# Optimization experiments

Measured on AMD Instinct MI355X. Metric: run time of the kernel, lower is better.

The kernel has to match this reference:

```python
import jax, jax.numpy as jnp
import numpy as np

N_Q_HEADS = 16
N_KV_HEADS = 4
HEAD_DIM = 64
GROUPS = N_Q_HEADS // N_KV_HEADS


def apply_rope(xq, xk, cos, sin):
    # xq: [B,S,Hq,D], xk: [B,S,Hkv,D]; cos/sin: [S, D/2]
    def rot(t):
        tr = t[..., 0::2]
        ti = t[..., 1::2]
        c = cos[None, :, None, :]
        s = sin[None, :, None, :]
        out_r = tr * c - ti * s
        out_i = tr * s + ti * c
        # interleave back: [..., D/2, 2] -> [..., D]
        return jnp.stack([out_r, out_i], axis=-1).reshape(t.shape)
    return rot(xq), rot(xk)


def setup_inputs() -> dict:
    key = jax.random.key(0)
    ks = jax.random.split(key, 8)
    B, S, DIM = 2, 2048, 1024
    x = jax.random.normal(ks[0], (B, S, DIM), jnp.float32)
    # RoPE frequencies (llama-style): theta_i = 10000^(-2i/D), angles = pos * theta
    inv_freq = 1.0 / (10000.0 ** (jnp.arange(0, HEAD_DIM, 2, dtype=jnp.float32) / HEAD_DIM))
    angles = jnp.arange(S, dtype=jnp.float32)[:, None] * inv_freq[None, :]  # [S, D/2]
    freqs_cos = jnp.cos(angles)
    freqs_sin = jnp.sin(angles)
    # additive causal mask [1,1,S,S]
    neg = jnp.float32(-1e9)
    mask = jnp.where(jnp.tril(jnp.ones((S, S), bool)), 0.0, neg)[None, None]
    scale = 0.02
    wq = jax.random.normal(ks[1], (DIM, N_Q_HEADS * HEAD_DIM), jnp.float32) * scale
    wk = jax.random.normal(ks[2], (DIM, N_KV_HEADS * HEAD_DIM), jnp.float32) * scale
    wv = jax.random.normal(ks[3], (DIM, N_KV_HEADS * HEAD_DIM), jnp.float32) * scale
    wo = jax.random.normal(ks[4], (DIM, DIM), jnp.float32) * scale
    return {"x": x, "start_pos": 0, "freqs_cos": freqs_cos, "freqs_sin": freqs_sin,
            "mask": mask, "wq": wq, "wk": wk, "wv": wv, "wo": wo}


def reference(x, start_pos, freqs_cos, freqs_sin, mask, wq, wk, wv, wo):
    B, S, DIM = x.shape
    xq = (x @ wq).reshape(B, S, N_Q_HEADS, HEAD_DIM)
    xk = (x @ wk).reshape(B, S, N_KV_HEADS, HEAD_DIM)
    xv = (x @ wv).reshape(B, S, N_KV_HEADS, HEAD_DIM)
    xq, xk = apply_rope(xq, xk, freqs_cos, freqs_sin)
    # seq_len > 1: prefill path, no KV-cache read. repeat_kv: expand kv heads by GROUPS.
    keys = jnp.repeat(xk, GROUPS, axis=2)    # [B,S,Hq,D]
    values = jnp.repeat(xv, GROUPS, axis=2)
    q = xq.transpose(0, 2, 1, 3)             # [B,H,S,D]
    k = keys.transpose(0, 2, 1, 3)
    v = values.transpose(0, 2, 1, 3)
    scores = jnp.einsum('bhqd,bhkd->bhqk', q, k) / jnp.sqrt(jnp.float32(HEAD_DIM))
    scores = scores + mask
    probs = jax.nn.softmax(scores, axis=-1)
    attn = jnp.einsum('bhqk,bhkd->bhqd', probs, v)  # [B,H,S,D]
    attn = attn.transpose(0, 2, 1, 3).reshape(B, S, DIM)
    return attn @ wo
```

## Files before the change

kernel.cpp:

```cpp
#include <hip/hip_runtime.h>

typedef __bf16 bf16_t;
typedef __bf16 bf16x8 __attribute__((ext_vector_type(8)));
typedef __bf16 bf16x4 __attribute__((ext_vector_type(4)));
typedef float f32x4 __attribute__((ext_vector_type(4)));
typedef short short4v __attribute__((ext_vector_type(4)));

#if __has_builtin(__builtin_amdgcn_exp2f)
#define EXP2F __builtin_amdgcn_exp2f
#else
#define EXP2F exp2f
#endif

#define BATCH 2
#define SEQ   2048
#define DIM   1024
#define NQH   16
#define NKVH  4
#define HD    64
#define ROWS  (BATCH*SEQ)
#define QKVN  1536
#define QSCALE 0.1803368801111f

static __device__ __forceinline__ short4v as_s4(bf16x4 v) {
    union { bf16x4 b; short4v s; } u; u.b = v; return u.s;
}

static __device__ __forceinline__ void gld16(const bf16_t* g, bf16_t* l) {
    __builtin_amdgcn_global_load_lds((const __attribute__((address_space(1))) void*)g,
                                     (__attribute__((address_space(3))) void*)l,
                                     16, 0, 0);
}

__global__ __launch_bounds__(256) void cast_x_kernel(const float* __restrict__ x,
                                                     bf16_t* __restrict__ o) {
    size_t i = ((size_t)blockIdx.x * 256 + threadIdx.x) * 4;
    float4 v = *(const float4*)(x + i);
    bf16x4 r;
    r[0] = (bf16_t)v.x; r[1] = (bf16_t)v.y; r[2] = (bf16_t)v.z; r[3] = (bf16_t)v.w;
    *(bf16x4*)(o + i) = r;
}

__global__ __launch_bounds__(256) void transpose_w_all(const float* __restrict__ wq,
                                                       const float* __restrict__ wk,
                                                       const float* __restrict__ wv,
                                                       const float* __restrict__ wo,
                                                       bf16_t* __restrict__ WqkvT,
                                                       bf16_t* __restrict__ WoT) {
    int bid = blockIdx.x;
    const float* src; bf16_t* dst; int N, nt, kt2;
    if (bid < 256)      { src = wq; dst = WqkvT;                      N = 1024; int i = bid;       nt = i & 15; kt2 = i >> 4; }
    else if (bid < 320) { src = wk; dst = WqkvT + (size_t)1024*1024;  N = 256;  int i = bid - 256; nt = i & 3;  kt2 = i >> 2; }
    else if (bid < 384) { src = wv; dst = WqkvT + (size_t)1280*1024;  N = 256;  int i = bid - 320; nt = i & 3;  kt2 = i >> 2; }
    else                { src = wo; dst = WoT;                        N = 1024; int i = bid - 384; nt = i & 15; kt2 = i >> 4; }

    __shared__ float tile[64][65];
    int t = threadIdx.x;
    {
        int r = t >> 2, cb = (t & 3) * 16;
        const float* s = src + (size_t)(kt2 * 64 + r) * N + nt * 64 + cb;
#pragma unroll
        for (int j = 0; j < 16; j += 4) {
            float4 v = *(const float4*)(s + j);
            tile[r][cb + j + 0] = v.x; tile[r][cb + j + 1] = v.y;
            tile[r][cb + j + 2] = v.z; tile[r][cb + j + 3] = v.w;
        }
    }
    __syncthreads();
    {
        int n = t >> 2, kb = (t & 3) * 16;
        union { bf16_t h[16]; uint4 u[2]; } pk;
#pragma unroll
        for (int j = 0; j < 16; ++j) pk.h[j] = (bf16_t)tile[kb + j][n];
        bf16_t* d = dst + (size_t)(nt * 64 + n) * 1024 + kt2 * 64 + kb;
        ((uint4*)d)[0] = pk.u[0];
        ((uint4*)d)[1] = pk.u[1];
    }
}

__global__ __launch_bounds__(256, 3) void gemm_qkv_kernel(const bf16_t* __restrict__ A,
                                                          const bf16_t* __restrict__ Bt,
                                                          const float* __restrict__ fcos,
                                                          const float* __restrict__ fsin,
                                                          bf16_t* __restrict__ Qb,
                                                          bf16_t* __restrict__ Kb,
                                                          bf16_t* __restrict__ Vt) {
    const int K = 1024;
    __shared__ __align__(16) bf16_t As[64 * 64];
    __shared__ __align__(16) bf16_t Bs[128 * 64];
    int t = threadIdx.x;
    int w = t >> 6, L = t & 63, quad = L >> 4, l15 = L & 15;
    int wr = (w >> 1) * 32, wc = (w & 1) * 64;

    int xid = blockIdx.x;
    int sw = (xid & 7) * 96 + (xid >> 3);
    int bnb = sw % 12;
    int bm = (sw / 12) * 64, bn = bnb * 128;

    int srow = L >> 3;
    int schunk = (L & 7) ^ srow;
    const bf16_t* Ag = A  + (size_t)(bm + w * 16 + srow) * K + schunk * 8;
    const bf16_t* Bg = Bt + (size_t)(bn + w * 32 + srow) * K + schunk * 8;
    bf16_t* Al = As + w * 1024;
    bf16_t* Bl = Bs + w * 2048;

    int rs0 = quad ^ (l15 & 7);
    int rs1 = (4 + quad) ^ (l15 & 7);

    f32x4 acc[2][4] = {};

    for (int k0 = 0; k0 < K; k0 += 64) {
        __syncthreads();
        gld16(Ag + k0,                 Al);
        gld16(Ag + (size_t)8 * K + k0, Al + 512);
#pragma unroll
        for (int c = 0; c < 4; ++c)
            gld16(Bg + (size_t)(c * 8) * K + k0, Bl + c * 512);
        __syncthreads();

#pragma unroll
        for (int kk = 0; kk < 2; ++kk) {
            int rsl = kk ? rs1 : rs0;
            bf16x8 a[2], b[4];
#pragma unroll
            for (int i = 0; i < 2; ++i)
                a[i] = ((const bf16x8*)As)[(wr + 16 * i + l15) * 8 + rsl];
#pragma unroll
            for (int j = 0; j < 4; ++j)
                b[j] = ((const bf16x8*)Bs)[(wc + 16 * j + l15) * 8 + rsl];
#pragma unroll
            for (int i = 0; i < 2; ++i)
#pragma unroll
                for (int j = 0; j < 4; ++j)
                    acc[i][j] = __builtin_amdgcn_mfma_f32_16x16x32_bf16(a[i], b[j], acc[i][j], 0, 0, 0);
        }
    }

    int region = (bnb >= 10) ? 2 : (bnb >= 8) ? 1 : 0;
#pragma unroll
    for (int i = 0; i < 2; ++i) {
        int row0 = bm + wr + 16 * i + quad * 4;
        int b = row0 >> 11, s0 = row0 & 2047;
#pragma unroll
        for (int j = 0; j < 4; ++j) {
            int col = bn + wc + 16 * j + l15;
            if (region == 2) {
                int kvh = (col >> 6) - 20, d = col & 63;
                bf16x4 o;
#pragma unroll
                for (int r = 0; r < 4; ++r) o[r] = (bf16_t)acc[i][j][r];
                *(bf16x4*)(Vt + ((size_t)((b * NKVH + kvh) * HD + d)) * SEQ + s0) = o;
            } else {
                int d = col & 63, fi = d >> 1;
                int odd = col & 1;
#pragma unroll
                for (int r = 0; r < 4; ++r) {
                    int s = s0 + r;
                    float v = acc[i][j][r];
                    float p = __shfl_xor(v, 1);
                    float c = fcos[s * 32 + fi], sn = fsin[s * 32 + fi];
                    float o = odd ? (p * sn + v * c) : (v * c - p * sn);
                    if (region == 0) {
                        int h = col >> 6;
                        Qb[((size_t)((b * NQH + h) * SEQ + s)) * HD + d] = (bf16_t)(o * QSCALE);
                    } else {
                        int kvh = (col >> 6) - 16;
                        Kb[((size_t)((b * NKVH + kvh) * SEQ + s)) * HD + d] = (bf16_t)o;
                    }
                }
            }
        }
    }
}

__global__ __launch_bounds__(256, 2) void gemm_bt_kernel(const bf16_t* __restrict__ A,
                                                         const bf16_t* __restrict__ Bt,
                                                         float* __restrict__ C) {
    const int K = 1024, N = 1024;
    __shared__ __align__(16) bf16_t As[64 * 64];
    __shared__ __align__(16) bf16_t Bs[128 * 64];
    int t = threadIdx.x;
    int w = t >> 6, L = t & 63, quad = L >> 4, l15 = L & 15;
    int wr = (w >> 1) * 32, wc = (w & 1) * 64;

    int xid = blockIdx.x;
    int sw = (xid & 7) * 64 + (xid >> 3);
    int bm = (sw >> 3) * 64, bn = (sw & 7) * 128;

    int srow = L >> 3;
    int schunk = (L & 7) ^ srow;
    const bf16_t* Ag = A  + (size_t)(bm + w * 16 + srow) * K + schunk * 8;
    const bf16_t* Bg = Bt + (size_t)(bn + w * 32 + srow) * K + schunk * 8;
    bf16_t* Al = As + w * 1024;
    bf16_t* Bl = Bs + w * 2048;

    int rs0 = quad ^ (l15 & 7);
    int rs1 = (4 + quad) ^ (l15 & 7);

    f32x4 acc[2][4] = {};

    for (int k0 = 0; k0 < K; k0 += 64) {
        __syncthreads();
        gld16(Ag + k0,                 Al);
        gld16(Ag + (size_t)8 * K + k0, Al + 512);
#pragma unroll
        for (int c = 0; c < 4; ++c)
            gld16(Bg + (size_t)(c * 8) * K + k0, Bl + c * 512);
        __syncthreads();

#pragma unroll
        for (int kk = 0; kk < 2; ++kk) {
            int rsl = kk ? rs1 : rs0;
            bf16x8 a[2], b[4];
#pragma unroll
            for (int i = 0; i < 2; ++i)
                a[i] = ((const bf16x8*)As)[(wr + 16 * i + l15) * 8 + rsl];
#pragma unroll
            for (int j = 0; j < 4; ++j)
                b[j] = ((const bf16x8*)Bs)[(wc + 16 * j + l15) * 8 + rsl];
#pragma unroll
            for (int i = 0; i < 2; ++i)
#pragma unroll
                for (int j = 0; j < 4; ++j)
                    acc[i][j] = __builtin_amdgcn_mfma_f32_16x16x32_bf16(a[i], b[j], acc[i][j], 0, 0, 0);
        }
    }

#pragma unroll
    for (int i = 0; i < 2; ++i) {
        int row = bm + wr + 16 * i + quad * 4;
#pragma unroll
        for (int j = 0; j < 4; ++j) {
            int col = bn + wc + 16 * j + l15;
            float* cp = C + (size_t)row * N + col;
#pragma unroll
            for (int r = 0; r < 4; ++r)
                cp[(size_t)r * N] = acc[i][j][r];
        }
    }
}

__global__ __launch_bounds__(256, 3) void attn_kernel(const bf16_t* __restrict__ Qb,
                                                      const bf16_t* __restrict__ Kb,
                                                      const bf16_t* __restrict__ Vt,
                                                      bf16_t* __restrict__ Ob) {
    int id = blockIdx.x;
    int sw = (id & 7) * 64 + (id >> 3);
    int b  = sw >> 8;
    int kv = (sw >> 6) & 3;
    int h  = kv * 4 + ((sw >> 4) & 3);
    int p  = sw & 15;

    int t = threadIdx.x, w = t >> 6, lane = t & 63, quad = lane >> 4, l15 = lane & 15;

    __shared__ __align__(16) bf16_t Ks[128 * 64];
    __shared__ __align__(16) bf16_t Vs[2][64 * 128];

    const bf16_t* Qbase = Qb + ((size_t)(b * NQH + h)) * SEQ * HD;
    const bf16_t* Kbase = Kb + ((size_t)(b * NKVH + kv)) * SEQ * HD;
    const bf16_t* Vbase = Vt + ((size_t)(b * NKVH + kv)) * HD * SEQ;

    const bf16_t* kS0 = Kbase + (size_t)(t >> 3) * HD + (size_t)(((t & 7) ^ ((t >> 3) & 7)) * 8);
    const bf16_t* vS0 = Vbase + (size_t)(t >> 4) * SEQ + (size_t)(((t & 15) ^ ((t >> 4) & 7)) * 8);
    int ldso = w * 512;

#pragma unroll 1
    for (int ph = 0; ph < 2; ++ph) {
        int qt = ph ? (31 - p) : p;
        int wq = qt * 64 + 16 * w + l15;
        int ktmax = qt >> 1;

        bf16x8 aq[2];
#pragma unroll
        for (int ks = 0; ks < 2; ++ks)
            aq[ks] = *(const bf16x8*)(Qbase + (size_t)wq * HD + ks * 32 + quad * 8);

        f32x4 acc_o[4] = {};
        float rs = 0.f;

        __syncthreads();
#pragma unroll
        for (int j = 0; j < 4; ++j) {
            gld16(kS0 + (size_t)j * 32 * HD, Ks + ldso + j * 2048);
            gld16(vS0 + (size_t)j * 16 * SEQ, Vs[0] + ldso + j * 2048);
        }

        int cur = 0;
        for (int kt = 0; kt <= ktmax; ++kt) {
            __syncthreads();
            if (kt < ktmax) {
                const bf16_t* vp = vS0 + (size_t)(kt + 1) * 128;
                bf16_t* vd = Vs[cur ^ 1] + ldso;
#pragma unroll
                for (int j = 0; j < 4; ++j)
                    gld16(vp + (size_t)j * 16 * SEQ, vd + j * 2048);
            }

            short4v bp[8];
            if (kt == ktmax) {
                int kb = kt * 128 + quad * 4;
#pragma unroll
                for (int x = 0; x < 8; ++x) {
                    int key = 16 * x + l15;
                    bf16x8 ak0 = ((const bf16x8*)Ks)[key * 8 + ((0 + quad) ^ (key & 7))];
                    bf16x8 ak1 = ((const bf16x8*)Ks)[key * 8 + ((4 + quad) ^ (key & 7))];
                    f32x4 z = {0.f, 0.f, 0.f, 0.f};
                    z = __builtin_amdgcn_mfma_f32_16x16x32_bf16(ak0, aq[0], z, 0, 0, 0);
                    z = __builtin_amdgcn_mfma_f32_16x16x32_bf16(ak1, aq[1], z, 0, 0, 0);
                    bf16x4 pb;
#pragma unroll
                    for (int r = 0; r < 4; ++r) {
                        float pv = (kb + 16 * x + r <= wq) ? EXP2F(z[r]) : 0.f;
                        rs += pv; pb[r] = (bf16_t)pv;
                    }
                    bp[x] = as_s4(pb);
                }
            } else {
#pragma unroll
                for (int x = 0; x < 8; ++x) {
                    int key = 16 * x + l15;
                    bf16x8 ak0 = ((const bf16x8*)Ks)[key * 8 + ((0 + quad) ^ (key & 7))];
                    bf16x8 ak1 = ((const bf16x8*)Ks)[key * 8 + ((4 + quad) ^ (key & 7))];
                    f32x4 z = {0.f, 0.f, 0.f, 0.f};
                    z = __builtin_amdgcn_mfma_f32_16x16x32_bf16(ak0, aq[0], z, 0, 0, 0);
                    z = __builtin_amdgcn_mfma_f32_16x16x32_bf16(ak1, aq[1], z, 0, 0, 0);
                    bf16x4 pb;
#pragma unroll
                    for (int r = 0; r < 4; ++r) {
                        float pv = EXP2F(z[r]);
                        rs += pv; pb[r] = (bf16_t)pv;
                    }
                    bp[x] = as_s4(pb);
                }
            }

            if (kt < ktmax) {
                __syncthreads();
                const bf16_t* kp = kS0 + (size_t)(kt + 1) * 128 * HD;
#pragma unroll
                for (int j = 0; j < 4; ++j)
                    gld16(kp + (size_t)j * 32 * HD, Ks + ldso + j * 2048);
            }

            __builtin_amdgcn_s_setprio(1);
#pragma unroll
            for (int dt = 0; dt < 4; ++dt) {
                int d = 16 * dt + l15;
#pragma unroll
                for (int x = 0; x < 8; ++x) {
                    int pos = (2 * x + (quad >> 1)) ^ (d & 7);
                    bf16x4 av = *(const bf16x4*)(Vs[cur] + d * 128 + pos * 8 + (quad & 1) * 4);
                    acc_o[dt] = __builtin_amdgcn_mfma_f32_16x16x16bf16_1k(as_s4(av), bp[x], acc_o[dt], 0, 0, 0);
                }
            }
            __builtin_amdgcn_s_setprio(0);
            cur ^= 1;
        }

        rs += __shfl_xor(rs, 16);
        rs += __shfl_xor(rs, 32);
        float rinv = 1.0f / rs;
        bf16_t* obase = Ob + (size_t)(b * SEQ + wq) * DIM + h * HD;
#pragma unroll
        for (int dt = 0; dt < 4; ++dt) {
            bf16x4 o;
#pragma unroll
            for (int r = 0; r < 4; ++r) o[r] = (bf16_t)(acc_o[dt][r] * rinv);
            *(bf16x4*)(obase + 16 * dt + quad * 4) = o;
        }
    }
}

extern "C" void kernel_launch(void* const* d_in, const int* in_sizes, int n_in,
                              void* d_out, int out_size, void* d_ws, size_t ws_size,
                              hipStream_t stream) {
    const float* x    = (const float*)d_in[0];
    const float* fcos = (const float*)d_in[2];
    const float* fsin = (const float*)d_in[3];
    const float* wq   = (const float*)d_in[5];
    const float* wk   = (const float*)d_in[6];
    const float* wv   = (const float*)d_in[7];
    const float* wo   = (const float*)d_in[8];
    float* out = (float*)d_out;

    char* ws = (char*)d_ws;
    bf16_t* Xb    = (bf16_t*)(ws + 0);
    bf16_t* Attnb = Xb;
    bf16_t* WqkvT = (bf16_t*)(ws + 8388608);
    bf16_t* WoT   = (bf16_t*)(ws + 11534336);
    bf16_t* Qb    = (bf16_t*)(ws + 13631488);
    bf16_t* Kb    = (bf16_t*)(ws + 22020096);
    bf16_t* Vt    = (bf16_t*)(ws + 24117248);

    cast_x_kernel<<<ROWS * DIM / 1024, 256, 0, stream>>>(x, Xb);
    transpose_w_all<<<640, 256, 0, stream>>>(wq, wk, wv, wo, WqkvT, WoT);

    gemm_qkv_kernel<<<(QKVN / 128) * (ROWS / 64), 256, 0, stream>>>(Xb, WqkvT, fcos, fsin, Qb, Kb, Vt);

    attn_kernel<<<512, 256, 0, stream>>>(Qb, Kb, Vt, Attnb);

    gemm_bt_kernel<<<(DIM / 128) * (ROWS / 64), 256, 0, stream>>>(Attnb, WoT, out);
}
```

Baseline: 168.4 us.

## Split attention keys across waves with cross-wave LDS reduction and double-buffered K

```diff
diff --git a/kernel.cpp b/kernel.cpp
--- a/kernel.cpp
+++ b/kernel.cpp
@@ -240,7 +240,7 @@
     }
 }
 
-__global__ __launch_bounds__(256, 3) void attn_kernel(const bf16_t* __restrict__ Qb,
+__global__ __launch_bounds__(256, 2) void attn_kernel(const bf16_t* __restrict__ Qb,
                                                       const bf16_t* __restrict__ Kb,
                                                       const bf16_t* __restrict__ Vt,
                                                       bf16_t* __restrict__ Ob) {
@@ -253,8 +253,11 @@
 
     int t = threadIdx.x, w = t >> 6, lane = t & 63, quad = lane >> 4, l15 = lane & 15;
 
-    __shared__ __align__(16) bf16_t Ks[128 * 64];
-    __shared__ __align__(16) bf16_t Vs[2][64 * 128];
+    __shared__ __align__(16) char smem[69632];
+    __shared__ float rsw[4][64];
+    bf16_t* KsBuf = (bf16_t*)smem;
+    bf16_t* VsBuf = (bf16_t*)smem + 16384;
+    float*  red   = (float*)smem;
 
     const bf16_t* Qbase = Qb + ((size_t)(b * NQH + h)) * SEQ * HD;
     const bf16_t* Kbase = Kb + ((size_t)(b * NKVH + kv)) * SEQ * HD;
@@ -267,106 +270,147 @@
 #pragma unroll 1
     for (int ph = 0; ph < 2; ++ph) {
         int qt = ph ? (31 - p) : p;
-        int wq = qt * 64 + 16 * w + l15;
+        int Q0 = qt * 64;
         int ktmax = qt >> 1;
 
-        bf16x8 aq[2];
-#pragma unroll
-        for (int ks = 0; ks < 2; ++ks)
-            aq[ks] = *(const bf16x8*)(Qbase + (size_t)wq * HD + ks * 32 + quad * 8);
-
-        f32x4 acc_o[4] = {};
-        float rs = 0.f;
-
-        __syncthreads();
-#pragma unroll
-        for (int j = 0; j < 4; ++j) {
-            gld16(kS0 + (size_t)j * 32 * HD, Ks + ldso + j * 2048);
-            gld16(vS0 + (size_t)j * 16 * SEQ, Vs[0] + ldso + j * 2048);
+        bf16x8 aq[4][2];
+#pragma unroll
+        for (int j = 0; j < 4; ++j)
+#pragma unroll
+            for (int ks = 0; ks < 2; ++ks)
+                aq[j][ks] = *(const bf16x8*)(Qbase + (size_t)(Q0 + 16 * j + l15) * HD + ks * 32 + quad * 8);
+
+        f32x4 acc[4][4] = {};
+        float rs[4] = {};
+
+        __syncthreads();
+#pragma unroll
+        for (int j4 = 0; j4 < 4; ++j4) {
+            gld16(kS0 + (size_t)j4 * 32 * HD,  KsBuf + ldso + j4 * 2048);
+            gld16(vS0 + (size_t)j4 * 16 * SEQ, VsBuf + ldso + j4 * 2048);
         }
 
         int cur = 0;
         for (int kt = 0; kt <= ktmax; ++kt) {
             __syncthreads();
             if (kt < ktmax) {
+                const bf16_t* kp = kS0 + (size_t)(kt + 1) * 128 * HD;
                 const bf16_t* vp = vS0 + (size_t)(kt + 1) * 128;
-                bf16_t* vd = Vs[cur ^ 1] + ldso;
-#pragma unroll
-                for (int j = 0; j < 4; ++j)
-                    gld16(vp + (size_t)j * 16 * SEQ, vd + j * 2048);
-            }
-
-            short4v bp[8];
-            if (kt == ktmax) {
-                int kb = kt * 128 + quad * 4;
-#pragma unroll
-                for (int x = 0; x < 8; ++x) {
-                    int key = 16 * x + l15;
-                    bf16x8 ak0 = ((const bf16x8*)Ks)[key * 8 + ((0 + quad) ^ (key & 7))];
-                    bf16x8 ak1 = ((const bf16x8*)Ks)[key * 8 + ((4 + quad) ^ (key & 7))];
-                    f32x4 z = {0.f, 0.f, 0.f, 0.f};
-                    z = __builtin_amdgcn_mfma_f32_16x16x32_bf16(ak0, aq[0], z, 0, 0, 0);
-                    z = __builtin_amdgcn_mfma_f32_16x16x32_bf16(ak1, aq[1], z, 0, 0, 0);
-                    bf16x4 pb;
-#pragma unroll
-                    for (int r = 0; r < 4; ++r) {
-                        float pv = (kb + 16 * x + r <= wq) ? EXP2F(z[r]) : 0.f;
-                        rs += pv; pb[r] = (bf16_t)pv;
-                    }
-                    bp[x] = as_s4(pb);
-                }
-            } else {
-#pragma unroll
-                for (int x = 0; x < 8; ++x) {
-                    int key = 16 * x + l15;
-                    bf16x8 ak0 = ((const bf16x8*)Ks)[key * 8 + ((0 + quad) ^ (key & 7))];
-                    bf16x8 ak1 = ((const bf16x8*)Ks)[key * 8 + ((4 + quad) ^ (key & 7))];
-                    f32x4 z = {0.f, 0.f, 0.f, 0.f};
-                    z = __builtin_amdgcn_mfma_f32_16x16x32_bf16(ak0, aq[0], z, 0, 0, 0);
-                    z = __builtin_amdgcn_mfma_f32_16x16x32_bf16(ak1, aq[1], z, 0, 0, 0);
-                    bf16x4 pb;
-#pragma unroll
-                    for (int r = 0; r < 4; ++r) {
-                        float pv = EXP2F(z[r]);
-                        rs += pv; pb[r] = (bf16_t)pv;
-                    }
-                    bp[x] = as_s4(pb);
+                bf16_t* kd = KsBuf + (cur ^ 1) * 8192 + ldso;
+                bf16_t* vd = VsBuf + (cur ^ 1) * 8192 + ldso;
+#pragma unroll
+                for (int j4 = 0; j4 < 4; ++j4) {
+                    gld16(kp + (size_t)j4 * 32 * HD,  kd + j4 * 2048);
+                    gld16(vp + (size_t)j4 * 16 * SEQ, vd + j4 * 2048);
                 }
             }
-
-            if (kt < ktmax) {
-                __syncthreads();
-                const bf16_t* kp = kS0 + (size_t)(kt + 1) * 128 * HD;
+            const bf16_t* KsC = KsBuf + cur * 8192;
+            const bf16_t* VsC = VsBuf + cur * 8192;
+
+            if (!(kt == ktmax && !(qt & 1) && w >= 2)) {
+                short4v bp[2][4];
+                if (kt == ktmax) {
+#pragma unroll
+                    for (int g2 = 0; g2 < 2; ++g2) {
+                        int g = 2 * w + g2;
+                        int keyl = 16 * g + l15;
+                        bf16x8 ak0 = ((const bf16x8*)KsC)[keyl * 8 + (quad ^ (keyl & 7))];
+                        bf16x8 ak1 = ((const bf16x8*)KsC)[keyl * 8 + ((4 + quad) ^ (keyl & 7))];
+                        int kb = kt * 128 + 16 * g + quad * 4;
+#pragma unroll
+                        for (int j = 0; j < 4; ++j) {
+                            f32x4 z = {0.f, 0.f, 0.f, 0.f};
+                            z = __builtin_amdgcn_mfma_f32_16x16x32_bf16(ak0, aq[j][0], z, 0, 0, 0);
+                            z = __builtin_amdgcn_mfma_f32_16x16x32_bf16(ak1, aq[j][1], z, 0, 0, 0);
+                            int qrow = Q0 + 16 * j + l15;
+                            bf16x4 pb;
+#pragma unroll
+                            for (int r = 0; r < 4; ++r) {
+                                float pv = (kb + r <= qrow) ? EXP2F(z[r]) : 0.f;
+                                rs[j] += pv; pb[r] = (bf16_t)pv;
+                            }
+                            bp[g2][j] = as_s4(pb);
+                        }
+                    }
+                } else {
+#pragma unroll
+                    for (int g2 = 0; g2 < 2; ++g2) {
+                        int g = 2 * w + g2;
+                        int keyl = 16 * g + l15;
+                        bf16x8 ak0 = ((const bf16x8*)KsC)[keyl * 8 + (quad ^ (keyl & 7))];
+                        bf16x8 ak1 = ((const bf16x8*)KsC)[keyl * 8 + ((4 + quad) ^ (keyl & 7))];
+#pragma unroll
+                        for (int j = 0; j < 4; ++j) {
+                            f32x4 z = {0.f, 0.f, 0.f, 0.f};
+                            z = __builtin_amdgcn_mfma_f32_16x16x32_bf16(ak0, aq[j][0], z, 0, 0, 0);
+                            z = __builtin_amdgcn_mfma_f32_16x16x32_bf16(ak1, aq[j][1], z, 0, 0, 0);
+                            bf16x4 pb;
+#pragma unroll
+                            for (int r = 0; r < 4; ++r) {
+                                float pv = EXP2F(z[r]);
+                                rs[j] += pv; pb[r] = (bf16_t)pv;
+                            }
+                            bp[g2][j] = as_s4(pb);
+                        }
+                    }
+                }
+
+                __builtin_amdgcn_s_setprio(1);
+#pragma unroll
+                for (int dt = 0; dt < 4; ++dt) {
+                    int d = 16 * dt + l15;
+#pragma unroll
+                    for (int g2 = 0; g2 < 2; ++g2) {
+                        int g = 2 * w + g2;
+                        int pos = (2 * g + (quad >> 1)) ^ (d & 7);
+                        bf16x4 av = *(const bf16x4*)(VsC + d * 128 + pos * 8 + (quad & 1) * 4);
+#pragma unroll
+                        for (int j = 0; j < 4; ++j)
+                            acc[dt][j] = __builtin_amdgcn_mfma_f32_16x16x16bf16_1k(as_s4(av), bp[g2][j], acc[dt][j], 0, 0, 0);
+                    }
+                }
+                __builtin_amdgcn_s_setprio(0);
+            }
+            cur ^= 1;
+        }
+
+        __syncthreads();
+        {
+            float* rw = red + w * 4352;
+#pragma unroll
+            for (int dt = 0; dt < 4; ++dt)
 #pragma unroll
                 for (int j = 0; j < 4; ++j)
-                    gld16(kp + (size_t)j * 32 * HD, Ks + ldso + j * 2048);
+                    *(f32x4*)(rw + (16 * j + l15) * 68 + 16 * dt + quad * 4) = acc[dt][j];
+        }
+#pragma unroll
+        for (int j = 0; j < 4; ++j) {
+            float v = rs[j];
+            v += __shfl_xor(v, 16);
+            v += __shfl_xor(v, 32);
+            if (quad == 0) rsw[w][16 * j + l15] = v;
+        }
+        __syncthreads();
+
+        {
+            int qg = Q0 + lane;
+            float rtot = rsw[0][lane] + rsw[1][lane] + rsw[2][lane] + rsw[3][lane];
+            float rinv = 1.0f / rtot;
+            union { bf16_t hh[16]; uint4 u[2]; } pk;
+#pragma unroll
+            for (int dq = 0; dq < 4; ++dq) {
+                f32x4 s = *(const f32x4*)(red + lane * 68 + 16 * w + 4 * dq);
+#pragma unroll
+                for (int w2 = 1; w2 < 4; ++w2) {
+                    f32x4 tp = *(const f32x4*)(red + w2 * 4352 + lane * 68 + 16 * w + 4 * dq);
+                    s[0] += tp[0]; s[1] += tp[1]; s[2] += tp[2]; s[3] += tp[3];
+                }
+#pragma unroll
+                for (int r = 0; r < 4; ++r) pk.hh[4 * dq + r] = (bf16_t)(s[r] * rinv);
             }
-
-            __builtin_amdgcn_s_setprio(1);
-#pragma unroll
-            for (int dt = 0; dt < 4; ++dt) {
-                int d = 16 * dt + l15;
-#pragma unroll
-                for (int x = 0; x < 8; ++x) {
-                    int pos = (2 * x + (quad >> 1)) ^ (d & 7);
-                    bf16x4 av = *(const bf16x4*)(Vs[cur] + d * 128 + pos * 8 + (quad & 1) * 4);
-                    acc_o[dt] = __builtin_amdgcn_mfma_f32_16x16x16bf16_1k(as_s4(av), bp[x], acc_o[dt], 0, 0, 0);
-                }
-            }
-            __builtin_amdgcn_s_setprio(0);
-            cur ^= 1;
-        }
-
-        rs += __shfl_xor(rs, 16);
-        rs += __shfl_xor(rs, 32);
-        float rinv = 1.0f / rs;
-        bf16_t* obase = Ob + (size_t)(b * SEQ + wq) * DIM + h * HD;
-#pragma unroll
-        for (int dt = 0; dt < 4; ++dt) {
-            bf16x4 o;
-#pragma unroll
-            for (int r = 0; r < 4; ++r) o[r] = (bf16_t)(acc_o[dt][r] * rinv);
-            *(bf16x4*)(obase + 16 * dt + quad * 4) = o;
+            bf16_t* ob = Ob + (size_t)(b * SEQ + qg) * DIM + h * HD + 16 * w;
+            ((uint4*)ob)[0] = pk.u[0];
+            ((uint4*)ob)[1] = pk.u[1];
         }
     }
 }
```

New measurement: 167.1 us. About the same (-0.8%).
